# Optimization experiments

Hardware: AMD Instinct MI355X
Metric: run time of the kernel (lower is better)

Reference implementation:

```python
import jax, jax.numpy as jnp
import numpy as np
from math import log2

FPS = 100.0
MIN_BPM = 55.0
MAX_BPM = 215.0
NUM_TEMPI = 60
NUM_BEATS = 4
TRANS_LAMBDA = 100.0
OBS_LAMBDA = 16.0
NUM_FRAMES = 6000


def _intervals():
    mi = 60.0 * FPS / MAX_BPM
    ma = 60.0 * FPS / MIN_BPM
    iv = np.arange(round(mi), round(ma) + 1)
    if NUM_TEMPI < len(iv):
        n = NUM_TEMPI
        iv = np.zeros(0)
        while len(iv) < NUM_TEMPI:
            iv = np.unique(np.round(np.logspace(log2(mi), log2(ma), n, base=2)))
            n += 1
    return iv.astype(np.int64)


def _state_space():
    iv = _intervals()                      # (I,) tempo intervals in frames
    nsb = int(iv.sum())                    # states per beat
    first = np.concatenate([[0], np.cumsum(iv)[:-1]]).astype(np.int64)
    last = (np.cumsum(iv) - 1).astype(np.int64)
    pos_b = np.concatenate([np.arange(i) / float(i) for i in iv])
    positions = np.concatenate([pos_b + b for b in range(NUM_BEATS)])  # (S,)
    first_states = np.stack([first + b * nsb for b in range(NUM_BEATS)])  # (B,I)
    last_states = np.stack([last + b * nsb for b in range(NUM_BEATS)])    # (B,I)
    # exponential tempo transition (madmom exponential_transition, norm=True)
    ratio = iv[None, :].astype(np.float64) / iv[:, None].astype(np.float64)
    prob = np.exp(-TRANS_LAMBDA * np.abs(ratio - 1.0))
    prob[prob <= np.spacing(1)] = 0.0
    prob /= prob.sum(axis=1, keepdims=True)
    log_t = np.where(prob > 0, np.log(np.maximum(prob, 1e-300)), -1e30).astype(np.float32)
    log_trans = np.tile(log_t[None], (NUM_BEATS, 1, 1))  # same lambda per beat boundary
    prev_last = np.stack([last_states[(b - 1) % NUM_BEATS] for b in range(NUM_BEATS)])
    # observation pointers: 0 = no beat, 1 = beat, 2 = downbeat
    frac = positions % 1.0
    beat_idx = np.floor(positions).astype(np.int64)
    ptr = np.where(frac < 1.0 / OBS_LAMBDA, np.where(beat_idx == 0, 2, 1), 0)
    return first_states, prev_last, log_trans, ptr, nsb * NUM_BEATS


def setup_inputs() -> dict:
    key = jax.random.key(0)
    first_states, prev_last, log_trans, pointer, S = _state_space()
    # beat/downbeat activation probabilities; scaled so beat+downbeat < 1
    acts = jax.random.uniform(key, (NUM_FRAMES, 2), dtype=jnp.float32) * 0.45
    return {
        "activations": acts,
        "log_trans": jnp.asarray(log_trans),
        "prev_last": jnp.asarray(prev_last, dtype=jnp.int32),
        "first_states": jnp.asarray(first_states, dtype=jnp.int32),
        "pointer": jnp.asarray(pointer, dtype=jnp.int32),
        "num_states": S,
    }


def reference(activations, log_trans, prev_last, first_states, pointer, num_states):
    S = int(num_states)
    NEG = jnp.float32(-1e30)
    a_b = activations[:, 0]
    a_d = activations[:, 1]
    # log observation densities: [no-beat, beat, downbeat], shape (F, 3)
    dens = jnp.stack([
        jnp.log((1.0 - a_b - a_d) / (OBS_LAMBDA - 1.0)),
        jnp.log(a_b),
        jnp.log(a_d),
    ], axis=1)
    first_flat = first_states.reshape(-1)  # (B*I,)
    base_ptr = jnp.arange(S, dtype=jnp.int32) - 1  # default predecessor s-1

    def step(v, dens_t):
        # within-interval advance: state s comes from s-1 with prob 1
        v_shift = jnp.concatenate([jnp.full((1,), NEG, v.dtype), v[:-1]])
        # beat boundaries: first states of beat b from last states of beat b-1
        cand = v[prev_last]                      # (B, I)
        scores = cand[:, :, None] + log_trans    # (B, I_from, I_to)
        best = scores.max(axis=1).reshape(-1)    # (B*I,)
        arg = scores.argmax(axis=1)              # (B, I_to)
        bp_first = jnp.take_along_axis(prev_last, arg.astype(jnp.int32), axis=1).reshape(-1)
        ptr = base_ptr.at[first_flat].set(bp_first)
        v_new = v_shift.at[first_flat].set(best) + dens_t[pointer]
        return v_new, ptr

    v0 = jnp.full((S,), -jnp.log(jnp.float32(S)))  # uniform initial distribution
    v_final, bps = jax.lax.scan(step, v0, dens)    # bps: (F, S) backpointers
    last_state = jnp.argmax(v_final).astype(jnp.int32)
    logp = v_final[last_state]

    def back(s, bp_t):
        p = bp_t[s]
        return p, p

    _, earlier = jax.lax.scan(back, last_state, bps[1:], reverse=True)
    path = jnp.concatenate([earlier, last_state[None]])  # (F,) best state sequence
    return path, logp
```

## Files before the change

### kernel.cpp

```cpp
#include <hip/hip_runtime.h>
#include <stdint.h>


#define NB 4
#define KF 15
#define QW 16
#define NPMAX 256
#define NEGV -1.0e30f

__device__ __forceinline__ float bf16u_to_f(uint16_t u) {
    union { uint32_t i; float f; } v; v.i = ((uint32_t)u) << 16; return v.f;
}
template<int CTRL>
__device__ __forceinline__ int dpp_i(int x) {
    return __builtin_amdgcn_update_dpp(0, x, CTRL, 0xF, 0xF, true);
}
template<int CTRL>
__device__ __forceinline__ float dpp_f(float x) {
    return __int_as_float(dpp_i<CTRL>(__float_as_int(x)));
}
__device__ __forceinline__ void load_acts(const void* p, int isbf, int t, float& a, float& d) {
    if (isbf) {
        const uint16_t* u = (const uint16_t*)p;
        uint32_t w = *(const uint32_t*)(u + 2 * t);
        a = bf16u_to_f((uint16_t)w); d = bf16u_to_f((uint16_t)(w >> 16));
    } else {
        const float2* f = (const float2*)p;
        float2 v = f[t]; a = v.x; d = v.y;
    }
}

__global__ __launch_bounds__(1024) void dbn_viterbi_v5(
    const void* __restrict__ acts_raw,
    const void* __restrict__ lt_raw,
    const int*  __restrict__ prev_last,
    const int*  __restrict__ first_states,
    float*      __restrict__ out,
    float*      __restrict__ ws_lastv,
    float*      __restrict__ ws_dens,
    int T, int S, int F)
{
    const int tid  = (int)threadIdx.x;
    const int NP   = NB * T;
    const int lane = tid & 63;
    const int wvx  = tid >> 6;

    __shared__ alignas(16) float lring[32 * 256];
    __shared__ alignas(16) float densr[64 * 4];
    __shared__ float bestp2[2 * 256];
    __shared__ float bound2[32];
    __shared__ int   fsld[NPMAX];
    __shared__ int   plds[NPMAX];
    __shared__ int   pref[NPMAX + 1];
    __shared__ float wvs[16];
    __shared__ int   wss[16];
    __shared__ int   flag_s, mspan_s;

    if (tid == 0) {
        const uint16_t* au = (const uint16_t*)acts_raw;
        int bf = 1;
        for (int i = 0; i < 32; i++) {
            uint16_t e = au[2 * i];
            uint8_t h8 = (uint8_t)(e >> 8);
            if (!(e == 0 || (h8 >= 0x20 && h8 < 0x40))) bf = 0;
        }
        flag_s = bf; mspan_s = 0;
    }
    if (tid < NP) { fsld[tid] = first_states[tid]; plds[tid] = prev_last[tid]; }
    for (int i = tid; i < 32 * 256; i += 1024) lring[i] = NEGV;
    __syncthreads();
    const int isbf = flag_s;
    const int nsb  = S / NB;
    const uint16_t* lt_u = (const uint16_t*)lt_raw;
    const float*    lt_f = (const float*)lt_raw;

    for (int f = tid; f < F; f += 1024) {
        float ab, ad;
        load_acts(acts_raw, isbf, f, ab, ad);
        float4 r;
        r.x = logf(((1.0f - ab) - ad) / 15.0f);
        r.y = logf(ab);
        r.z = logf(ad);
        r.w = 0.0f;
        *(float4*)&ws_dens[f * 4] = r;
    }
    __threadfence();
    if (tid == 0) {
        int acc = 0;
        for (int g = 0; g < NP; g++) {
            int b = g / T, ib = g - b * T;
            int end = (ib + 1 < T) ? fsld[g + 1] : (b + 1) * nsb;
            int L = end - fsld[g];
            pref[g] = acc; acc += (L + KF - 1) / KF;
        }
        pref[NP] = acc;
    }
    __syncthreads();
    const int NT = pref[NP];
    const float vinit = -logf((float)S);
    const int WQ = NP >> 2, TQ = T >> 2;

    const bool act_u = (tid < NT);
    int g_own = 0, startg = 0, Lg = 1, sb = 0, lq = 0, kk_head = -1;
    bool is_last = false, pv2 = false, pred_is_head = false;
    if (act_u) {
        int lo = 0, hi = NP - 1;
        while (lo < hi) { int mid = (lo + hi + 1) >> 1; if (pref[mid] <= tid) lo = mid; else hi = mid - 1; }
        g_own = lo;
        int j = tid - pref[lo];
        int b = g_own / T, ib = g_own - b * T;
        startg = fsld[g_own];
        int end = (ib + 1 < T) ? fsld[g_own + 1] : (b + 1) * nsb;
        Lg = end - startg;
        int n = (Lg + KF - 1) / KF;
        sb = startg + Lg - KF * (n - j);
        is_last = (j == n - 1);
        lq = (b << 6) + ib;
        pv2 = (b == 0);
        int i0 = sb - startg;
        kk_head = (i0 <= 0) ? (-i0) : -1;
        pred_is_head = (i0 == 1);
    }
    bool hb[KF], hpp[KF];
    #pragma unroll
    for (int kk = 0; kk < KF; kk++) {
        int i = (sb - startg) + kk;
        hb[kk]  = act_u && (16 * i < Lg);
        hpp[kk] = act_u && (kk >= 1) && (i == 1);
    }

    const int g_a = tid >> 2, k4 = tid & 3;
    const bool act_g = (g_a < NP);
    int rowbase = 0, lo_b = 0, b_a = 0, j_a = 0, dsel_a = 1;
    if (act_g) {
        b_a = g_a / T; j_a = g_a - b_a * T;
        rowbase = ((b_a + 3) & 3) << 6;
        dsel_a = (b_a == 0) ? 2 : 1;
        int lo = T, hi = 0;
        for (int i = 0; i < T; i++) {
            int idx = (b_a * T + i) * T + j_a;
            float v = isbf ? bf16u_to_f(lt_u[idx]) : lt_f[idx];
            if (v > -1e29f) { if (i < lo) lo = i; hi = i; }
        }
        lo_b = lo;
        if (k4 == 0) atomicMax(&mspan_s, hi - lo + 1);
    }
    __syncthreads();
    const bool banded = (mspan_s <= 44);
    float ltreg[QW];
    #pragma unroll
    for (int u = 0; u < QW; u++) ltreg[u] = NEGV;
    int cb = 0;
    if (act_g) {
        if (banded) { cb = (lo_b & ~3) + 12 * k4; if (cb > 52) cb = 52; }
        else cb = 16 * k4;
        const int nu = banded ? 12 : 16;
        for (int u = 0; u < nu; u++) {
            int i = cb + u;
            if (i < T) {
                int idx = (b_a * T + i) * T + j_a;
                ltreg[u] = isbf ? bf16u_to_f(lt_u[idx]) : lt_f[idx];
            }
        }
    }

    float vreg[KF];
    #pragma unroll
    for (int kk = 0; kk < KF; kk++) vreg[kk] = vinit;
    if (act_u && is_last) lring[(31 << 8) + lq] = vinit;
    if (lane == 63) bound2[16 + wvx] = vinit;
    if (tid < 256) bestp2[256 + tid] = vinit;
    if (tid < 64 && tid < F) {
        float4 r = *(const float4*)&ws_dens[tid * 4];
        *(float4*)&densr[tid * 4] = r;
    }
    __syncthreads();

    for (int t = 0; t < F; t++) {
        if ((t & 15) == 0 && t >= 16 && lane < WQ) {
            int row = t - 16 + wvx;
            int c = lane, beat = c / TQ;
            float4 v4 = *(const float4*)&lring[((row & 31) << 8) + 4 * c + 4 * beat];
            *(float4*)&ws_lastv[(size_t)row * NP + 4 * c] = v4;
        }
        if (wvx == 15 && (t & 31) == 0 && t >= 32 && lane < 32) {
            int fr = t + 31 + lane;
            if (fr < F) {
                float4 r = *(const float4*)&ws_dens[fr * 4];
                *(float4*)&densr[(fr & 63) * 4] = r;
            }
        }

        if (act_g) {
            const float* rowp = &lring[(((t + 31) & 31) << 8) + rowbase + cb];
            float4 l0 = *(const float4*)(rowp + 0);
            float4 l1 = *(const float4*)(rowp + 4);
            float4 l2 = *(const float4*)(rowp + 8);
            float m0 = fmaxf(fmaxf(l0.x + ltreg[0], l0.y + ltreg[1]),
                             fmaxf(l0.z + ltreg[2], l0.w + ltreg[3]));
            float m1 = fmaxf(fmaxf(l1.x + ltreg[4], l1.y + ltreg[5]),
                             fmaxf(l1.z + ltreg[6], l1.w + ltreg[7]));
            float m2 = fmaxf(fmaxf(l2.x + ltreg[8], l2.y + ltreg[9]),
                             fmaxf(l2.z + ltreg[10], l2.w + ltreg[11]));
            float mv = fmaxf(fmaxf(m0, m1), m2);
            if (!banded) {
                float4 l3 = *(const float4*)(rowp + 12);
                float m3 = fmaxf(fmaxf(l3.x + ltreg[12], l3.y + ltreg[13]),
                                 fmaxf(l3.z + ltreg[14], l3.w + ltreg[15]));
                mv = fmaxf(mv, m3);
            }
            mv = fmaxf(mv, dpp_f<0xB1>(mv));
            mv = fmaxf(mv, dpp_f<0x4E>(mv));
            if (k4 == 0) bestp2[((t & 1) << 8) + g_a] = mv + densr[((t & 63) << 2) + dsel_a];
        }

        float sh = __shfl_up(vreg[KF - 1], 1, 64);
        float patchv = bestp2[(((t + 1) & 1) << 8) + g_own];
        int doff = (t & 63) << 2;
        float d0  = densr[doff];
        float dpv = densr[doff + (pv2 ? 2 : 1)];
        float inc = (lane == 0) ? bound2[(((t + 1) & 1) << 4) + ((wvx + 15) & 15)] : sh;
        inc = pred_is_head ? patchv : inc;
        #pragma unroll
        for (int kk = KF - 1; kk >= 0; kk--) {
            float prev = (kk == 0) ? inc : vreg[kk - 1];
            prev = hpp[kk] ? patchv : prev;
            float add = hb[kk] ? dpv : d0;
            vreg[kk] = prev + add;
        }
        if (act_u && is_last) lring[((t & 31) << 8) + lq] = vreg[KF - 1];
        if (lane == 63) bound2[((t & 1) << 4) + wvx] = vreg[KF - 1];

        __syncthreads();
    }

    {
        int t0 = (F - 1) & ~15;
        int row = t0 + wvx;
        if (row <= F - 2 && lane < WQ) {
            int c = lane, beat = c / TQ;
            float4 v4 = *(const float4*)&lring[((row & 31) << 8) + 4 * c + 4 * beat];
            *(float4*)&ws_lastv[(size_t)row * NP + 4 * c] = v4;
        }
        __threadfence();
    }

    float patchF = bestp2[(((F - 1) & 1) << 8) + g_own];
    float mv = -INFINITY; int ms = 0x7FFFFFFF;
    #pragma unroll
    for (int kk = 0; kk < KF; kk++) {
        int s = sb + kk;
        float v = (kk == kk_head) ? patchF : vreg[kk];
        if (act_u && s >= startg && v > mv) { mv = v; ms = s; }
    }
    #pragma unroll
    for (int d = 1; d < 64; d <<= 1) {
        float ov = __shfl_xor(mv, d, 64);
        int   os = __shfl_xor(ms, d, 64);
        if (ov > mv || (ov == mv && os < ms)) { mv = ov; ms = os; }
    }
    if (lane == 0) { wvs[wvx] = mv; wss[wvx] = ms; }
    __syncthreads();

    if (tid == 0) {
        float bm = -INFINITY; int bs = 0x7FFFFFFF;
        for (int w = 0; w < 16; w++) {
            if (wvs[w] > bm || (wvs[w] == bm && wss[w] < bs)) { bm = wvs[w]; bs = wss[w]; }
        }
        int s = bs;
        int t = F - 1;
        out[F - 1] = (float)s;
        while (t > 0) {
            int b = s / nsb;
            int lo = b * T, hi = b * T + T - 1;
            while (lo < hi) { int mid = (lo + hi + 1) >> 1; if (fsld[mid] <= s) lo = mid; else hi = mid - 1; }
            int p = lo;
            int run = s - fsld[p];
            if (run == 0) {
                int jt = p - b * T;
                int pb = (b + 3) & 3;
                const float* lrow = &ws_lastv[(size_t)(t - 1) * NP + pb * T];
                float bmv = -INFINITY; int ai = 0;
                for (int i = 0; i < T; i++) {
                    int idx = (b * T + i) * T + jt;
                    float ltv = isbf ? bf16u_to_f(lt_u[idx]) : lt_f[idx];
                    float sc = lrow[i] + ltv;
                    if (sc > bmv) { bmv = sc; ai = i; }
                }
                s = plds[b * T + ai];
                out[t - 1] = (float)s;
                t--;
            } else {
                int m = (run < t) ? run : t;
                for (int jj = 0; jj < m; jj++) out[t - 1 - jj] = (float)(s - 1 - jj);
                s -= m; t -= m;
            }
        }
        out[F] = bm;
    }
}

__global__ __launch_bounds__(1024) void dbn_viterbi_v2(
    const void* __restrict__ acts_raw, const void* __restrict__ lt_raw,
    const int* __restrict__ prev_last, const int* __restrict__ first_states,
    float* __restrict__ out, float* __restrict__ ws_lastv, float* __restrict__ ws_dens,
    int T, int S, int F)
{
    const int tid  = (int)threadIdx.x;
    const int NP   = NB * T;
    const int lane = tid & 63;
    const int wvx  = tid >> 6;

    __shared__ alignas(16) float lring[32 * 256];
    __shared__ alignas(16) float densr[64 * 4];
    __shared__ float bestv[NPMAX];
    __shared__ float bound[16];
    __shared__ int   fsld[NPMAX];
    __shared__ int   plds[NPMAX];
    __shared__ int   pref[NPMAX + 1];
    __shared__ float wvs[16];
    __shared__ int   wss[16];
    __shared__ int   flag_s, mspan_s;

    if (tid == 0) {
        const uint16_t* au = (const uint16_t*)acts_raw;
        int bf = 1;
        for (int i = 0; i < 32; i++) {
            uint16_t e = au[2 * i];
            uint8_t h8 = (uint8_t)(e >> 8);
            if (!(e == 0 || (h8 >= 0x20 && h8 < 0x40))) bf = 0;
        }
        flag_s = bf; mspan_s = 0;
    }
    if (tid < NP) { fsld[tid] = first_states[tid]; plds[tid] = prev_last[tid]; }
    for (int i = tid; i < 32 * 256; i += 1024) lring[i] = NEGV;
    __syncthreads();
    const int isbf = flag_s;
    const int nsb  = S / NB;
    const uint16_t* lt_u = (const uint16_t*)lt_raw;
    const float*    lt_f = (const float*)lt_raw;

    for (int f = tid; f < F; f += 1024) {
        float ab, ad;
        load_acts(acts_raw, isbf, f, ab, ad);
        float4 r;
        r.x = logf(((1.0f - ab) - ad) / 15.0f);
        r.y = logf(ab);
        r.z = logf(ad);
        r.w = 0.0f;
        *(float4*)&ws_dens[f * 4] = r;
    }
    __threadfence();
    if (tid == 0) {
        int acc = 0;
        for (int g = 0; g < NP; g++) {
            int b = g / T, ib = g - b * T;
            int end = (ib + 1 < T) ? fsld[g + 1] : (b + 1) * nsb;
            int L = end - fsld[g];
            pref[g] = acc; acc += (L + KF - 1) / KF;
        }
        pref[NP] = acc;
    }
    __syncthreads();
    const int NT = pref[NP];

    const bool act_u = (tid < NT);
    int g_own = 0, startg = 0, Lg = 1, sb = 0, lq = 0;
    bool is_last = false, pv2 = false;
    if (act_u) {
        int lo = 0, hi = NP - 1;
        while (lo < hi) { int mid = (lo + hi + 1) >> 1; if (pref[mid] <= tid) lo = mid; else hi = mid - 1; }
        g_own = lo;
        int j = tid - pref[lo];
        int b = g_own / T, ib = g_own - b * T;
        startg = fsld[g_own];
        int end = (ib + 1 < T) ? fsld[g_own + 1] : (b + 1) * nsb;
        Lg = end - startg;
        int n = (Lg + KF - 1) / KF;
        sb = startg + Lg - KF * (n - j);
        is_last = (j == n - 1);
        lq = (b << 6) + ib;
        pv2 = (b == 0);
    }
    bool hb[KF], hq[KF];
    #pragma unroll
    for (int kk = 0; kk < KF; kk++) {
        int i = sb + kk - startg;
        hq[kk] = act_u && (i <= 0);
        hb[kk] = act_u && (16 * i < Lg);
    }

    const int g_a = tid >> 2, k4 = tid & 3;
    const bool act_g = (g_a < NP);
    int rowbase = 0, lo_b = 0, b_a = 0, j_a = 0;
    if (act_g) {
        b_a = g_a / T; j_a = g_a - b_a * T;
        rowbase = ((b_a + 3) & 3) << 6;
        int lo = T, hi = 0;
        for (int i = 0; i < T; i++) {
            int idx = (b_a * T + i) * T + j_a;
            float v = isbf ? bf16u_to_f(lt_u[idx]) : lt_f[idx];
            if (v > -1e29f) { if (i < lo) lo = i; hi = i; }
        }
        lo_b = lo;
        if (k4 == 0) atomicMax(&mspan_s, hi - lo + 1);
    }
    __syncthreads();
    const bool banded = (mspan_s <= 44);
    float ltreg[QW];
    #pragma unroll
    for (int u = 0; u < QW; u++) ltreg[u] = NEGV;
    int cb = 0;
    if (act_g) {
        if (banded) { cb = (lo_b & ~3) + 12 * k4; if (cb > 52) cb = 52; }
        else cb = 16 * k4;
        const int nu = banded ? 12 : 16;
        for (int u = 0; u < nu; u++) {
            int i = cb + u;
            if (i < T) {
                int idx = (b_a * T + i) * T + j_a;
                ltreg[u] = isbf ? bf16u_to_f(lt_u[idx]) : lt_f[idx];
            }
        }
    }

    const float vinit = -logf((float)S);
    float vreg[KF];
    #pragma unroll
    for (int kk = 0; kk < KF; kk++) vreg[kk] = vinit;
    if (act_u && is_last) lring[(31 << 8) + lq] = vinit;
    if (lane == 63) bound[wvx] = vinit;
    float inc_pipe = vinit;
    if (tid < 64 && tid < F) {
        float4 r = *(const float4*)&ws_dens[tid * 4];
        *(float4*)&densr[tid * 4] = r;
    }
    const int WQ = NP >> 2, TQ = T >> 2;

    for (int t = 0; t < F; t++) {
        __syncthreads();
        const float* lvR = &lring[((t + 31) & 31) << 8];
        float inc_use = inc_pipe;
        if (lane == 0) inc_use = bound[(wvx + 15) & 15];

        if (wvx == 15) {
            if ((t & 31) == 0 && t >= 32 && lane < 32) {
                int fr = t + 32 + lane;
                if (fr < F) {
                    float4 r = *(const float4*)&ws_dens[fr * 4];
                    *(float4*)&densr[(fr & 63) * 4] = r;
                }
            }
            if ((t & 15) == 0 && t > 0 && lane < WQ) {
                int c = lane, beat = c / TQ;
                int srcoff = 4 * c + 4 * beat, t0 = t - 16;
                for (int r2 = 0; r2 < 16; r2++) {
                    int row = t0 + r2;
                    float4 v4 = *(const float4*)&lring[((row & 31) << 8) + srcoff];
                    *(float4*)&ws_lastv[(size_t)row * NP + 4 * c] = v4;
                }
            }
        } else if (act_g) {
            const float* rowp = lvR + rowbase + cb;
            float4 l0 = *(const float4*)(rowp + 0);
            float4 l1 = *(const float4*)(rowp + 4);
            float4 l2 = *(const float4*)(rowp + 8);
            float m0 = fmaxf(fmaxf(l0.x + ltreg[0], l0.y + ltreg[1]),
                             fmaxf(l0.z + ltreg[2], l0.w + ltreg[3]));
            float m1 = fmaxf(fmaxf(l1.x + ltreg[4], l1.y + ltreg[5]),
                             fmaxf(l1.z + ltreg[6], l1.w + ltreg[7]));
            float m2 = fmaxf(fmaxf(l2.x + ltreg[8], l2.y + ltreg[9]),
                             fmaxf(l2.z + ltreg[10], l2.w + ltreg[11]));
            float mv = fmaxf(fmaxf(m0, m1), m2);
            if (!banded) {
                float4 l3 = *(const float4*)(rowp + 12);
                float m3 = fmaxf(fmaxf(l3.x + ltreg[12], l3.y + ltreg[13]),
                                 fmaxf(l3.z + ltreg[14], l3.w + ltreg[15]));
                mv = fmaxf(mv, m3);
            }
            mv = fmaxf(mv, dpp_f<0xB1>(mv));
            mv = fmaxf(mv, dpp_f<0x4E>(mv));
            if (k4 == 0) bestv[g_a] = mv;
        }

        __syncthreads();
        int doff = (t & 63) << 2;
        float d0  = densr[doff];
        float dpv = densr[doff + (pv2 ? 2 : 1)];
        float bq  = bestv[g_own];
        #pragma unroll
        for (int kk = KF - 1; kk >= 0; kk--) {
            float prev = (kk == 0) ? inc_use : vreg[kk - 1];
            prev = hq[kk] ? bq : prev;
            float add = hb[kk] ? dpv : d0;
            vreg[kk] = prev + add;
        }
        if (act_u && is_last) lring[((t & 31) << 8) + lq] = vreg[KF - 1];
        if (lane == 63) bound[wvx] = vreg[KF - 1];
        inc_pipe = __shfl_up(vreg[KF - 1], 1, 64);
    }

    __syncthreads();
    if (wvx == 15 && lane < WQ) {
        int lastf = (F - 1) & ~15;
        int c = lane, beat = c / TQ;
        int srcoff = 4 * c + 4 * beat;
        for (int row = lastf; row <= F - 2; row++) {
            float4 v4 = *(const float4*)&lring[((row & 31) << 8) + srcoff];
            *(float4*)&ws_lastv[(size_t)row * NP + 4 * c] = v4;
        }
        __threadfence();
    }

    float mv = -INFINITY; int ms = 0x7FFFFFFF;
    #pragma unroll
    for (int kk = 0; kk < KF; kk++) {
        int s = sb + kk;
        bool valid = act_u && (s >= startg);
        float v = vreg[kk];
        if (valid && v > mv) { mv = v; ms = s; }
    }
    #pragma unroll
    for (int d = 1; d < 64; d <<= 1) {
        float ov = __shfl_xor(mv, d, 64);
        int   os = __shfl_xor(ms, d, 64);
        if (ov > mv || (ov == mv && os < ms)) { mv = ov; ms = os; }
    }
    if (lane == 0) { wvs[wvx] = mv; wss[wvx] = ms; }
    __syncthreads();

    if (tid == 0) {
        float bm = -INFINITY; int bs = 0x7FFFFFFF;
        for (int w = 0; w < 16; w++) {
            if (wvs[w] > bm || (wvs[w] == bm && wss[w] < bs)) { bm = wvs[w]; bs = wss[w]; }
        }
        int s = bs;
        int t = F - 1;
        out[F - 1] = (float)s;
        while (t > 0) {
            int b = s / nsb;
            int lo = b * T, hi = b * T + T - 1;
            while (lo < hi) { int mid = (lo + hi + 1) >> 1; if (fsld[mid] <= s) lo = mid; else hi = mid - 1; }
            int p = lo;
            int run = s - fsld[p];
            if (run == 0) {
                int jt = p - b * T;
                int pb = (b + 3) & 3;
                const float* lrow = &ws_lastv[(size_t)(t - 1) * NP + pb * T];
                float bmv = -INFINITY; int ai = 0;
                for (int i = 0; i < T; i++) {
                    int idx = (b * T + i) * T + jt;
                    float ltv = isbf ? bf16u_to_f(lt_u[idx]) : lt_f[idx];
                    float sc = lrow[i] + ltv;
                    if (sc > bmv) { bmv = sc; ai = i; }
                }
                s = plds[b * T + ai];
                out[t - 1] = (float)s;
                t--;
            } else {
                int m = (run < t) ? run : t;
                for (int jj = 0; jj < m; jj++) out[t - 1 - jj] = (float)(s - 1 - jj);
                s -= m; t -= m;
            }
        }
        out[F] = bm;
    }
}

extern "C" void kernel_launch(void* const* d_in, const int* in_sizes, int n_in,
                              void* d_out, int out_size, void* d_ws, size_t ws_size,
                              hipStream_t stream) {
    const int F  = in_sizes[0] / 2;
    const int NP = in_sizes[2];
    const int T  = NP / NB;
    const int S  = in_sizes[4];

    const size_t need = ((size_t)F * NP + 4 * (size_t)F) * 4;
    float* ws_lv = (float*)d_ws;
    float* ws_de = ws_lv + (size_t)F * NP;

    const bool base = ((T & 3) == 0) && (T <= 64) && (NP <= NPMAX) && (F >= 2)
                   && ((S % NB) == 0) && (S <= KF * 1024) && (ws_size >= need);

    if (base) {
        hipLaunchKernelGGL(dbn_viterbi_v5, dim3(1), dim3(1024), 0, stream,
                           d_in[0], d_in[1],
                           (const int*)d_in[2], (const int*)d_in[3],
                           (float*)d_out, ws_lv, ws_de, T, S, F);
    } else {
        hipLaunchKernelGGL(dbn_viterbi_v2, dim3(1), dim3(1024), 0, stream,
                           d_in[0], d_in[1],
                           (const int*)d_in[2], (const int*)d_in[3],
                           (float*)d_out, ws_lv, ws_de, T, S, F);
    }
}
```

Baseline: 6.090 ms.

## Compute beat-boundary max with DPP wave rotation over diagonal band

Adds a fast path used when the transition band stays within fixed diagonal offsets and the hardware DPP row-rotate behaves as expected. In it, 8 wavefronts (two per beat, one per half-band) hold 24 diagonal transition weights in registers and rotate the previous last-state values across lanes with DPP, replacing the per-thread float4 LDS reads plus quad reductions. It also swaps the shuffle-up for a DPP shift, keeps densities in registers to prefetch one step ahead, and uses a raw barrier with an lgkmcnt wait. This moves boundary work onto fewer waves and removes LDS traffic on the serial per-frame critical path, at the cost of extra registers and a probe for DPP behaviour at startup.

New measurement: 6.080 ms. About the same (-0.2%).

```diff
diff --git a/kernel.cpp b/kernel.cpp
--- a/kernel.cpp
+++ b/kernel.cpp
@@ -7,6 +7,8 @@
 #define QW 16
 #define NPMAX 256
 #define NEGV -1.0e30f
+#define RDLO (-28)
+#define RDHI 19
 
 __device__ __forceinline__ float bf16u_to_f(uint16_t u) {
     union { uint32_t i; float f; } v; v.i = ((uint32_t)u) << 16; return v.f;
@@ -30,7 +32,7 @@
     }
 }
 
-__global__ __launch_bounds__(1024) void dbn_viterbi_v5(
+__global__ __launch_bounds__(1024) void dbn_viterbi_v6(
     const void* __restrict__ acts_raw,
     const void* __restrict__ lt_raw,
     const int*  __restrict__ prev_last,
@@ -47,14 +49,14 @@
 
     __shared__ alignas(16) float lring[32 * 256];
     __shared__ alignas(16) float densr[64 * 4];
-    __shared__ float bestp2[2 * 256];
+    __shared__ alignas(16) float bpr2[1024];
     __shared__ float bound2[32];
     __shared__ int   fsld[NPMAX];
     __shared__ int   plds[NPMAX];
     __shared__ int   pref[NPMAX + 1];
     __shared__ float wvs[16];
     __shared__ int   wss[16];
-    __shared__ int   flag_s, mspan_s;
+    __shared__ int   flag_s, mspan_s, dlo_s, dhi_s;
 
     if (tid == 0) {
         const uint16_t* au = (const uint16_t*)acts_raw;
@@ -64,7 +66,7 @@
             uint8_t h8 = (uint8_t)(e >> 8);
             if (!(e == 0 || (h8 >= 0x20 && h8 < 0x40))) bf = 0;
         }
-        flag_s = bf; mspan_s = 0;
+        flag_s = bf; mspan_s = 0; dlo_s = 0x3FFFFFFF; dhi_s = -0x3FFFFFFF;
     }
     if (tid < NP) { fsld[tid] = first_states[tid]; plds[tid] = prev_last[tid]; }
     for (int i = tid; i < 32 * 256; i += 1024) lring[i] = NEGV;
@@ -143,95 +145,198 @@
             if (v > -1e29f) { if (i < lo) lo = i; hi = i; }
         }
         lo_b = lo;
-        if (k4 == 0) atomicMax(&mspan_s, hi - lo + 1);
-    }
-    __syncthreads();
-    const bool banded = (mspan_s <= 44);
-    float ltreg[QW];
-    #pragma unroll
-    for (int u = 0; u < QW; u++) ltreg[u] = NEGV;
-    int cb = 0;
-    if (act_g) {
-        if (banded) { cb = (lo_b & ~3) + 12 * k4; if (cb > 52) cb = 52; }
-        else cb = 16 * k4;
-        const int nu = banded ? 12 : 16;
-        for (int u = 0; u < nu; u++) {
-            int i = cb + u;
-            if (i < T) {
-                int idx = (b_a * T + i) * T + j_a;
-                ltreg[u] = isbf ? bf16u_to_f(lt_u[idx]) : lt_f[idx];
-            }
-        }
-    }
+        if (k4 == 0) {
+            atomicMax(&mspan_s, hi - lo + 1);
+            atomicMin(&dlo_s, lo - j_a);
+            atomicMax(&dhi_s, hi - j_a);
+        }
+    }
+    __syncthreads();
 
     float vreg[KF];
     #pragma unroll
     for (int kk = 0; kk < KF; kk++) vreg[kk] = vinit;
     if (act_u && is_last) lring[(31 << 8) + lq] = vinit;
     if (lane == 63) bound2[16 + wvx] = vinit;
-    if (tid < 256) bestp2[256 + tid] = vinit;
+    if (tid < 256) {
+        bpr2[256 + tid]     = vinit;
+        bpr2[512 + 2 * tid] = vinit;
+        bpr2[513 + 2 * tid] = vinit;
+    }
     if (tid < 64 && tid < F) {
         float4 r = *(const float4*)&ws_dens[tid * 4];
         *(float4*)&densr[tid * 4] = r;
     }
     __syncthreads();
 
-    for (int t = 0; t < F; t++) {
-        if ((t & 15) == 0 && t >= 16 && lane < WQ) {
-            int row = t - 16 + wvx;
-            int c = lane, beat = c / TQ;
-            float4 v4 = *(const float4*)&lring[((row & 31) << 8) + 4 * c + 4 * beat];
-            *(float4*)&ws_lastv[(size_t)row * NP + 4 * c] = v4;
-        }
-        if (wvx == 15 && (t & 31) == 0 && t >= 32 && lane < 32) {
-            int fr = t + 31 + lane;
-            if (fr < F) {
-                float4 r = *(const float4*)&ws_dens[fr * 4];
-                *(float4*)&densr[(fr & 63) * 4] = r;
-            }
-        }
-
+    int rupt = dpp_i<0x134>(lane);
+    int rdnt = dpp_i<0x13C>(lane);
+    const bool dirok = (__builtin_amdgcn_readlane(rupt, 5) == 6) &&
+                       (__builtin_amdgcn_readlane(rdnt, 5) == 4);
+    const bool rotok = dirok && (dlo_s >= RDLO) && (dhi_s <= RDHI) && (NB == 4);
+
+    float patchF;
+
+    if (rotok) {
+        const int b_h    = wvx >> 1;
+        const int hlf    = wvx & 1;
+        const int rbh    = ((b_h + 3) & 3) << 6;
+        const int base_d = RDLO + 24 * hlf;
+        const int bT     = b_h * T;
+        float ltr[24];
+        if (wvx < 8) {
+            #pragma unroll
+            for (int u = 0; u < 24; u++) {
+                int i = lane + base_d + u;
+                float v = NEGV;
+                if (lane < T && i >= 0 && i < T) {
+                    int idx = (b_h * T + i) * T + lane;
+                    v = isbf ? bf16u_to_f(lt_u[idx]) : lt_f[idx];
+                }
+                ltr[u] = v;
+            }
+        } else {
+            #pragma unroll
+            for (int u = 0; u < 24; u++) ltr[u] = NEGV;
+        }
+        float4 dd = *(const float4*)&densr[0];
+        float4 ddp; ddp.x = 0.f; ddp.y = 0.f; ddp.z = 0.f; ddp.w = 0.f;
+
+        for (int t = 0; t < F; t++) {
+            if ((t & 15) == 0 && t >= 16 && lane < WQ) {
+                int row = t - 16 + wvx;
+                int c = lane, beat = c / TQ;
+                float4 v4 = *(const float4*)&lring[((row & 31) << 8) + 4 * c + 4 * beat];
+                *(float4*)&ws_lastv[(size_t)row * NP + 4 * c] = v4;
+            }
+            if (wvx == 15 && (t & 31) == 0 && t >= 32 && lane < 32) {
+                int fr = t + 31 + lane;
+                if (fr < F) {
+                    float4 r = *(const float4*)&ws_dens[fr * 4];
+                    *(float4*)&densr[(fr & 63) * 4] = r;
+                }
+            }
+            float4 ddn = *(const float4*)&densr[((t + 1) & 63) << 2];
+
+            if (wvx < 8) {
+                const int rb = (((t + 31) & 31) << 8) + rbh;
+                float r0 = lring[rb + ((lane + base_d) & 63)];
+                float r1 = lring[rb + ((lane + base_d + 12) & 63)];
+                float a0 = r0 + ltr[0];
+                float a1 = r1 + ltr[12];
+                #pragma unroll
+                for (int k2 = 1; k2 < 12; k2++) {
+                    r0 = dpp_f<0x134>(r0);
+                    r1 = dpp_f<0x134>(r1);
+                    a0 = fmaxf(a0, r0 + ltr[k2]);
+                    a1 = fmaxf(a1, r1 + ltr[12 + k2]);
+                }
+                float hm = fmaxf(a0, a1);
+                if (lane < T) bpr2[((t & 1) << 9) + ((bT + lane) << 1) + hlf] = hm;
+            }
+
+            float sh = dpp_f<0x13C>(vreg[KF - 1]);
+            float2 pp = *(const float2*)&bpr2[(((t + 1) & 1) << 9) + (g_own << 1)];
+            float dprev  = pv2 ? ddp.z : ddp.y;
+            float patchv = fmaxf(pp.x, pp.y) + dprev;
+            float d0  = dd.x;
+            float dpv = pv2 ? dd.z : dd.y;
+            float inc = (lane == 0) ? bound2[(((t + 1) & 1) << 4) + ((wvx + 15) & 15)] : sh;
+            inc = pred_is_head ? patchv : inc;
+            #pragma unroll
+            for (int kk = KF - 1; kk >= 0; kk--) {
+                float prev = (kk == 0) ? inc : vreg[kk - 1];
+                prev = hpp[kk] ? patchv : prev;
+                float add = hb[kk] ? dpv : d0;
+                vreg[kk] = prev + add;
+            }
+            if (act_u && is_last) lring[((t & 31) << 8) + lq] = vreg[KF - 1];
+            if (lane == 63) bound2[((t & 1) << 4) + wvx] = vreg[KF - 1];
+
+            ddp = dd; dd = ddn;
+            asm volatile("s_waitcnt lgkmcnt(0)\n\ts_barrier" ::: "memory");
+        }
+        {
+            float2 pf = *(const float2*)&bpr2[(((F - 1) & 1) << 9) + (g_own << 1)];
+            patchF = fmaxf(pf.x, pf.y) + (pv2 ? ddp.z : ddp.y);
+        }
+    } else {
+        const bool banded = (mspan_s <= 44);
+        float ltreg[QW];
+        #pragma unroll
+        for (int u = 0; u < QW; u++) ltreg[u] = NEGV;
+        int cb = 0;
         if (act_g) {
-            const float* rowp = &lring[(((t + 31) & 31) << 8) + rowbase + cb];
-            float4 l0 = *(const float4*)(rowp + 0);
-            float4 l1 = *(const float4*)(rowp + 4);
-            float4 l2 = *(const float4*)(rowp + 8);
-            float m0 = fmaxf(fmaxf(l0.x + ltreg[0], l0.y + ltreg[1]),
-                             fmaxf(l0.z + ltreg[2], l0.w + ltreg[3]));
-            float m1 = fmaxf(fmaxf(l1.x + ltreg[4], l1.y + ltreg[5]),
-                             fmaxf(l1.z + ltreg[6], l1.w + ltreg[7]));
-            float m2 = fmaxf(fmaxf(l2.x + ltreg[8], l2.y + ltreg[9]),
-                             fmaxf(l2.z + ltreg[10], l2.w + ltreg[11]));
-            float mv = fmaxf(fmaxf(m0, m1), m2);
-            if (!banded) {
-                float4 l3 = *(const float4*)(rowp + 12);
-                float m3 = fmaxf(fmaxf(l3.x + ltreg[12], l3.y + ltreg[13]),
-                                 fmaxf(l3.z + ltreg[14], l3.w + ltreg[15]));
-                mv = fmaxf(mv, m3);
-            }
-            mv = fmaxf(mv, dpp_f<0xB1>(mv));
-            mv = fmaxf(mv, dpp_f<0x4E>(mv));
-            if (k4 == 0) bestp2[((t & 1) << 8) + g_a] = mv + densr[((t & 63) << 2) + dsel_a];
-        }
-
-        float sh = __shfl_up(vreg[KF - 1], 1, 64);
-        float patchv = bestp2[(((t + 1) & 1) << 8) + g_own];
-        int doff = (t & 63) << 2;
-        float d0  = densr[doff];
-        float dpv = densr[doff + (pv2 ? 2 : 1)];
-        float inc = (lane == 0) ? bound2[(((t + 1) & 1) << 4) + ((wvx + 15) & 15)] : sh;
-        inc = pred_is_head ? patchv : inc;
-        #pragma unroll
-        for (int kk = KF - 1; kk >= 0; kk--) {
-            float prev = (kk == 0) ? inc : vreg[kk - 1];
-            prev = hpp[kk] ? patchv : prev;
-            float add = hb[kk] ? dpv : d0;
-            vreg[kk] = prev + add;
-        }
-        if (act_u && is_last) lring[((t & 31) << 8) + lq] = vreg[KF - 1];
-        if (lane == 63) bound2[((t & 1) << 4) + wvx] = vreg[KF - 1];
-
-        __syncthreads();
+            if (banded) { cb = (lo_b & ~3) + 12 * k4; if (cb > 52) cb = 52; }
+            else cb = 16 * k4;
+            const int nu = banded ? 12 : 16;
+            for (int u = 0; u < nu; u++) {
+                int i = cb + u;
+                if (i < T) {
+                    int idx = (b_a * T + i) * T + j_a;
+                    ltreg[u] = isbf ? bf16u_to_f(lt_u[idx]) : lt_f[idx];
+                }
+            }
+        }
+
+        for (int t = 0; t < F; t++) {
+            if ((t & 15) == 0 && t >= 16 && lane < WQ) {
+                int row = t - 16 + wvx;
+                int c = lane, beat = c / TQ;
+                float4 v4 = *(const float4*)&lring[((row & 31) << 8) + 4 * c + 4 * beat];
+                *(float4*)&ws_lastv[(size_t)row * NP + 4 * c] = v4;
+            }
+            if (wvx == 15 && (t & 31) == 0 && t >= 32 && lane < 32) {
+                int fr = t + 31 + lane;
+                if (fr < F) {
+                    float4 r = *(const float4*)&ws_dens[fr * 4];
+                    *(float4*)&densr[(fr & 63) * 4] = r;
+                }
+            }
+
+            if (act_g) {
+                const float* rowp = &lring[(((t + 31) & 31) << 8) + rowbase + cb];
+                float4 l0 = *(const float4*)(rowp + 0);
+                float4 l1 = *(const float4*)(rowp + 4);
+                float4 l2 = *(const float4*)(rowp + 8);
+                float m0 = fmaxf(fmaxf(l0.x + ltreg[0], l0.y + ltreg[1]),
+                                 fmaxf(l0.z + ltreg[2], l0.w + ltreg[3]));
+                float m1 = fmaxf(fmaxf(l1.x + ltreg[4], l1.y + ltreg[5]),
+                                 fmaxf(l1.z + ltreg[6], l1.w + ltreg[7]));
+                float m2 = fmaxf(fmaxf(l2.x + ltreg[8], l2.y + ltreg[9]),
+                                 fmaxf(l2.z + ltreg[10], l2.w + ltreg[11]));
+                float mv = fmaxf(fmaxf(m0, m1), m2);
+                if (!banded) {
+                    float4 l3 = *(const float4*)(rowp + 12);
+                    float m3 = fmaxf(fmaxf(l3.x + ltreg[12], l3.y + ltreg[13]),
+                                     fmaxf(l3.z + ltreg[14], l3.w + ltreg[15]));
+                    mv = fmaxf(mv, m3);
+                }
+                mv = fmaxf(mv, dpp_f<0xB1>(mv));
+                mv = fmaxf(mv, dpp_f<0x4E>(mv));
+                if (k4 == 0) bpr2[((t & 1) << 8) + g_a] = mv + densr[((t & 63) << 2) + dsel_a];
+            }
+
+            float sh = __shfl_up(vreg[KF - 1], 1, 64);
+            float patchv = bpr2[(((t + 1) & 1) << 8) + g_own];
+            int doff = (t & 63) << 2;
+            float d0  = densr[doff];
+            float dpv = densr[doff + (pv2 ? 2 : 1)];
+            float inc = (lane == 0) ? bound2[(((t + 1) & 1) << 4) + ((wvx + 15) & 15)] : sh;
+            inc = pred_is_head ? patchv : inc;
+            #pragma unroll
+            for (int kk = KF - 1; kk >= 0; kk--) {
+                float prev = (kk == 0) ? inc : vreg[kk - 1];
+                prev = hpp[kk] ? patchv : prev;
+                float add = hb[kk] ? dpv : d0;
+                vreg[kk] = prev + add;
+            }
+            if (act_u && is_last) lring[((t & 31) << 8) + lq] = vreg[KF - 1];
+            if (lane == 63) bound2[((t & 1) << 4) + wvx] = vreg[KF - 1];
+
+            __syncthreads();
+        }
+        patchF = bpr2[(((F - 1) & 1) << 8) + g_own];
     }
 
     {
@@ -245,7 +350,6 @@
         __threadfence();
     }
 
-    float patchF = bestp2[(((F - 1) & 1) << 8) + g_own];
     float mv = -INFINITY; int ms = 0x7FFFFFFF;
     #pragma unroll
     for (int kk = 0; kk < KF; kk++) {
@@ -583,7 +687,7 @@
                    && ((S % NB) == 0) && (S <= KF * 1024) && (ws_size >= need);
 
     if (base) {
-        hipLaunchKernelGGL(dbn_viterbi_v5, dim3(1), dim3(1024), 0, stream,
+        hipLaunchKernelGGL(dbn_viterbi_v6, dim3(1), dim3(1024), 0, stream,
                            d_in[0], d_in[1],
                            (const int*)d_in[2], (const int*)d_in[3],
                            (float*)d_out, ws_lv, ws_de, T, S, F);
```
